# Optimization experiments

Measured on AMD Instinct MI355X. Metric: run time of the kernel, lower is better.

## Reference

```python
import jax, jax.numpy as jnp
import numpy as np

N_NODES = 50000
N_EDGES = 800000
D = 64           # node feature / hidden dim for all 5 GCN layers
NUM_GRAPHS = 512
FINAL_NEURON = 128
OUT_DIM = 1
NUM_LAYERS = 5


def setup_inputs() -> dict:
    key = jax.random.key(0)
    ks = jax.random.split(key, 20)
    inp = {}
    inp["x"] = jax.random.normal(ks[0], (N_NODES, D), dtype=jnp.float32)
    inp["edge_index"] = jax.random.randint(ks[1], (2, N_EDGES), 0, N_NODES)
    inp["batch"] = jnp.sort(jax.random.randint(ks[2], (N_NODES,), 0, NUM_GRAPHS))
    # GCNConv weights (Glorot-ish) and biases for 5 layers, all D->D
    for i in range(NUM_LAYERS):
        inp[f"W{i+1}"] = jax.random.normal(ks[3 + i], (D, D), dtype=jnp.float32) / np.sqrt(D)
        inp[f"b{i+1}"] = jnp.zeros((D,), dtype=jnp.float32)
    inp["fc1_W"] = jax.random.normal(ks[10], (D, FINAL_NEURON), dtype=jnp.float32) / np.sqrt(D)
    inp["fc1_b"] = jnp.zeros((FINAL_NEURON,), dtype=jnp.float32)
    inp["fc2_W"] = jax.random.normal(ks[11], (FINAL_NEURON, OUT_DIM), dtype=jnp.float32) / np.sqrt(FINAL_NEURON)
    inp["fc2_b"] = jnp.zeros((OUT_DIM,), dtype=jnp.float32)
    return inp


def _gcn_conv(h, src, dst, dinv, W, b):
    # PyG GCNConv: x' = D^{-1/2} (A + I) D^{-1/2} (h W) + b, deg includes self-loop
    hw = h @ W                                           # [N, D_out]
    norm_e = dinv[src] * dinv[dst]                       # [E]
    msg = hw[src] * norm_e[:, None]                      # gather + scale
    agg = jax.ops.segment_sum(msg, dst, num_segments=h.shape[0])
    agg = agg + (dinv * dinv)[:, None] * hw              # self-loop contribution
    return agg + b


def reference(x, edge_index, batch, W1, b1, W2, b2, W3, b3, W4, b4, W5, b5,
              fc1_W, fc1_b, fc2_W, fc2_b):
    src, dst = edge_index[0], edge_index[1]
    n = x.shape[0]
    # degree on A + I (in-degree at dst, plus 1 self-loop)
    deg = jax.ops.segment_sum(jnp.ones(src.shape[0], x.dtype), dst, num_segments=n) + 1.0
    dinv = jax.lax.rsqrt(deg)
    h = x
    for W, b in ((W1, b1), (W2, b2), (W3, b3), (W4, b4), (W5, b5)):
        h = jax.nn.relu(_gcn_conv(h, src, dst, dinv, W, b))
    # global_add_pool readout over graph ids
    g = jax.ops.segment_sum(h, batch, num_segments=NUM_GRAPHS)   # [G, D]
    g = jax.nn.relu(g @ fc1_W + fc1_b)
    return g @ fc2_W + fc2_b                                     # [G, 1]
```

## Files before the change

### kernel.cpp

```cpp
#include <hip/hip_runtime.h>
#include <hip/hip_fp16.h>

#define N_NODES 50000
#define N_EDGES 800000
#define D 64
#define NUM_GRAPHS 512
#define FINAL_NEURON 128
#define SCAN_NB ((N_NODES + 255) / 256)

#define BN 32
#define NB_GEMM ((N_NODES + BN - 1) / BN)
#define NB_EDGE ((N_EDGES + 255) / 256)
#define ZS 72
#define WS 72

typedef unsigned short ushort_t;
typedef _Float16 f16;
typedef __attribute__((ext_vector_type(8))) _Float16 f16x8;
typedef __attribute__((ext_vector_type(4))) float f32x4;

__device__ __forceinline__ float2 h2f(unsigned v) {
    __half2 h = *reinterpret_cast<__half2*>(&v);
    return __half22float2(h);
}

__device__ __forceinline__ void acc_add8(float4& a0, float4& a1, uint4 u) {
    float2 p;
    p = h2f(u.x); a0.x += p.x; a0.y += p.y;
    p = h2f(u.y); a0.z += p.x; a0.w += p.y;
    p = h2f(u.z); a1.x += p.x; a1.y += p.y;
    p = h2f(u.w); a1.z += p.x; a1.w += p.y;
}

__global__ void k_zero1(int* a, int n) {
    int i = blockIdx.x * blockDim.x + threadIdx.x;
    if (i < n) a[i] = 0;
}

__global__ void k_hist(const int* __restrict__ dst, int* cnt, ushort_t* __restrict__ epos) {
    int e = blockIdx.x * blockDim.x + threadIdx.x;
    if (e < N_EDGES) epos[e] = (ushort_t)atomicAdd(&cnt[dst[e]], 1);
}

__global__ void k_blocksum(const int* __restrict__ cnt, int* __restrict__ bsum,
                           float* __restrict__ dinv, float* __restrict__ g) {
    __shared__ int sdata[256];
    int t = threadIdx.x;
    int i = blockIdx.x * 256 + t;
    int v = (i < N_NODES) ? cnt[i] : 0;
    if (i < N_NODES) dinv[i] = rsqrtf((float)v + 1.0f);
    if (i < NUM_GRAPHS * D) g[i] = 0.f;
    sdata[t] = v;
    __syncthreads();
    for (int s = 128; s > 0; s >>= 1) {
        if (t < s) sdata[t] += sdata[t + s];
        __syncthreads();
    }
    if (t == 0) bsum[blockIdx.x] = sdata[0];
}

__global__ void k_scanbsum(const int* __restrict__ bsum, int* __restrict__ boff) {
    __shared__ int buf[256];
    int t = threadIdx.x;
    int v = (t < SCAN_NB) ? bsum[t] : 0;
    buf[t] = v;
    __syncthreads();
    for (int off = 1; off < 256; off <<= 1) {
        int a = (t >= off) ? buf[t - off] : 0;
        __syncthreads();
        buf[t] += a;
        __syncthreads();
    }
    if (t < SCAN_NB) boff[t] = buf[t] - v;
}

__global__ void k_localscan(const int* __restrict__ cnt, const int* __restrict__ boff,
                            int* __restrict__ row) {
    __shared__ int buf[256];
    int t = threadIdx.x;
    int i = blockIdx.x * 256 + t;
    int v = (i < N_NODES) ? cnt[i] : 0;
    buf[t] = v;
    __syncthreads();
    for (int off = 1; off < 256; off <<= 1) {
        int a = (t >= off) ? buf[t - off] : 0;
        __syncthreads();
        buf[t] += a;
        __syncthreads();
    }
    if (i < N_NODES) row[i] = boff[blockIdx.x] + buf[t] - v;
    if (i == 0) row[N_NODES] = N_EDGES;
}

__device__ __forceinline__ void stage_wT(const float* __restrict__ W,
                                         f16* WhiT, f16* WloT, int t) {
    for (int idx = t; idx < D * D; idx += 256) {
        int k = idx >> 6, j = idx & 63;
        float w = W[idx];
        f16 hi = (f16)w;
        f16 lo = (f16)(w - (float)hi);
        WhiT[j * WS + k] = hi;
        WloT[j * WS + k] = lo;
    }
}

__device__ __forceinline__ void gather_node(const int* __restrict__ row,
                                            const ushort_t* __restrict__ esrc,
                                            const uint4* __restrict__ hp,
                                            int n, int q, float4& a0, float4& a1) {
    int e = row[n], e1 = row[n + 1];
    acc_add8(a0, a1, hp[(size_t)n * 8 + q]);
    if (e + 4 <= e1) {
        int i0 = __builtin_nontemporal_load(esrc + e);
        int i1 = __builtin_nontemporal_load(esrc + e + 1);
        int i2 = __builtin_nontemporal_load(esrc + e + 2);
        int i3 = __builtin_nontemporal_load(esrc + e + 3);
        do {
            uint4 u0 = hp[(size_t)i0 * 8 + q];
            uint4 u1 = hp[(size_t)i1 * 8 + q];
            uint4 u2 = hp[(size_t)i2 * 8 + q];
            uint4 u3 = hp[(size_t)i3 * 8 + q];
            e += 4;
            i0 = __builtin_nontemporal_load(esrc + e);
            i1 = __builtin_nontemporal_load(esrc + e + 1);
            i2 = __builtin_nontemporal_load(esrc + e + 2);
            i3 = __builtin_nontemporal_load(esrc + e + 3);
            acc_add8(a0, a1, u0); acc_add8(a0, a1, u1);
            acc_add8(a0, a1, u2); acc_add8(a0, a1, u3);
        } while (e + 4 <= e1);
    }
    for (; e < e1; ++e) {
        int s = __builtin_nontemporal_load(esrc + e);
        acc_add8(a0, a1, hp[(size_t)s * 8 + q]);
    }
}

__device__ __forceinline__ void gemm_32x64(const f16* zsh, const f16* WhiT, const f16* WloT,
                                           const float* dinvsh, f16* ysh, int t) {
    int w = t >> 6, l = t & 63;
    int rt = (w >> 1) * 16;
    int cb = (w & 1) * 32;
    int lr = l & 15, lg = l >> 4;
    f32x4 acc0 = {0.f, 0.f, 0.f, 0.f}, acc1 = {0.f, 0.f, 0.f, 0.f};
#pragma unroll
    for (int ks = 0; ks < 2; ++ks) {
        f16x8 a   = *(const f16x8*)&zsh [(rt + lr)      * ZS + ks * 32 + lg * 8];
        f16x8 bh0 = *(const f16x8*)&WhiT[(cb + lr)      * WS + ks * 32 + lg * 8];
        f16x8 bl0 = *(const f16x8*)&WloT[(cb + lr)      * WS + ks * 32 + lg * 8];
        f16x8 bh1 = *(const f16x8*)&WhiT[(cb + 16 + lr) * WS + ks * 32 + lg * 8];
        f16x8 bl1 = *(const f16x8*)&WloT[(cb + 16 + lr) * WS + ks * 32 + lg * 8];
        acc0 = __builtin_amdgcn_mfma_f32_16x16x32_f16(a, bh0, acc0, 0, 0, 0);
        acc0 = __builtin_amdgcn_mfma_f32_16x16x32_f16(a, bl0, acc0, 0, 0, 0);
        acc1 = __builtin_amdgcn_mfma_f32_16x16x32_f16(a, bh1, acc1, 0, 0, 0);
        acc1 = __builtin_amdgcn_mfma_f32_16x16x32_f16(a, bl1, acc1, 0, 0, 0);
    }
#pragma unroll
    for (int r = 0; r < 4; ++r) {
        int rrow = rt + lg * 4 + r;
        float s = dinvsh[rrow];
        ysh[rrow * ZS + cb + lr]      = (f16)(acc0[r] * s);
        ysh[rrow * ZS + cb + 16 + lr] = (f16)(acc1[r] * s);
    }
}

__global__ __launch_bounds__(256, 5)
void k_transform0(const float* __restrict__ x, const float* __restrict__ dinv,
                  const float* __restrict__ W1, __half* __restrict__ hout,
                  const int* __restrict__ src, const int* __restrict__ dst,
                  const int* __restrict__ row, const ushort_t* __restrict__ epos,
                  ushort_t* __restrict__ esrc) {
    int t = threadIdx.x;
    if (blockIdx.x >= NB_GEMM) {
        int e = (blockIdx.x - NB_GEMM) * 256 + t;
        if (e < N_EDGES) esrc[row[dst[e]] + (int)epos[e]] = (ushort_t)src[e];
        return;
    }
    __shared__ __attribute__((aligned(16))) f16 WhiT[D * WS];
    __shared__ __attribute__((aligned(16))) f16 WloT[D * WS];
    __shared__ __attribute__((aligned(16))) f16 zsh[BN * ZS];
    __shared__ __attribute__((aligned(16))) f16 ysh[BN * ZS];
    __shared__ float dinvsh[BN];
    int base = blockIdx.x * BN;
    stage_wT(W1, WhiT, WloT, t);
    if (t < BN) dinvsh[t] = (base + t < N_NODES) ? dinv[base + t] : 0.f;

    int nl = t >> 3, q = t & 7;
    int n = base + nl;
    float4 xa = {0,0,0,0}, xb = {0,0,0,0};
    if (n < N_NODES) {
        xa = ((const float4*)x)[(size_t)n * 16 + q * 2];
        xb = ((const float4*)x)[(size_t)n * 16 + q * 2 + 1];
    }
    f16x8 zv;
    zv[0] = (f16)xa.x; zv[1] = (f16)xa.y; zv[2] = (f16)xa.z; zv[3] = (f16)xa.w;
    zv[4] = (f16)xb.x; zv[5] = (f16)xb.y; zv[6] = (f16)xb.z; zv[7] = (f16)xb.w;
    *(f16x8*)&zsh[nl * ZS + q * 8] = zv;
    __syncthreads();
    gemm_32x64(zsh, WhiT, WloT, dinvsh, ysh, t);
    __syncthreads();
    if (n < N_NODES) {
        uint4 o = *(const uint4*)&ysh[nl * ZS + q * 8];
        ((uint4*)hout)[(size_t)n * 8 + q] = o;
    }
}

__global__ __launch_bounds__(256, 5)
void k_layer(const int* __restrict__ row, const ushort_t* __restrict__ esrc,
             const __half* __restrict__ hin, const float* __restrict__ dinv,
             const float* __restrict__ bias, const float* __restrict__ Wn,
             __half* __restrict__ hout) {
    __shared__ __attribute__((aligned(16))) f16 WhiT[D * WS];
    __shared__ __attribute__((aligned(16))) f16 WloT[D * WS];
    __shared__ __attribute__((aligned(16))) f16 zsh[BN * ZS];
    __shared__ __attribute__((aligned(16))) f16 ysh[BN * ZS];
    __shared__ float dinvsh[BN];
    int t = threadIdx.x;
    int base = blockIdx.x * BN;
    stage_wT(Wn, WhiT, WloT, t);
    if (t < BN) dinvsh[t] = (base + t < N_NODES) ? dinv[base + t] : 0.f;

    int nl = t >> 3, q = t & 7;
    int n = base + nl;
    float4 a0 = {0,0,0,0}, a1 = {0,0,0,0};
    float s = 0.f;
    if (n < N_NODES) {
        gather_node(row, esrc, (const uint4*)hin, n, q, a0, a1);
        s = dinv[n];
    }
    float4 b0 = ((const float4*)bias)[2 * q];
    float4 b1 = ((const float4*)bias)[2 * q + 1];
    f16x8 zv;
    zv[0] = (f16)fmaxf(a0.x * s + b0.x, 0.f);
    zv[1] = (f16)fmaxf(a0.y * s + b0.y, 0.f);
    zv[2] = (f16)fmaxf(a0.z * s + b0.z, 0.f);
    zv[3] = (f16)fmaxf(a0.w * s + b0.w, 0.f);
    zv[4] = (f16)fmaxf(a1.x * s + b1.x, 0.f);
    zv[5] = (f16)fmaxf(a1.y * s + b1.y, 0.f);
    zv[6] = (f16)fmaxf(a1.z * s + b1.z, 0.f);
    zv[7] = (f16)fmaxf(a1.w * s + b1.w, 0.f);
    *(f16x8*)&zsh[nl * ZS + q * 8] = zv;
    __syncthreads();
    gemm_32x64(zsh, WhiT, WloT, dinvsh, ysh, t);
    __syncthreads();
    if (n < N_NODES) {
        uint4 o = *(const uint4*)&ysh[nl * ZS + q * 8];
        ((uint4*)hout)[(size_t)n * 8 + q] = o;
    }
}

__global__ __launch_bounds__(256, 8)
void k_layer_pool(const int* __restrict__ row, const ushort_t* __restrict__ esrc,
                  const __half* __restrict__ hin, const float* __restrict__ dinv,
                  const float* __restrict__ bias, const int* __restrict__ batch,
                  float* __restrict__ g) {
    __shared__ float zf[BN * 65];
    __shared__ int bsh[BN];
    int t = threadIdx.x;
    int base = blockIdx.x * BN;
    if (t < BN) bsh[t] = (base + t < N_NODES) ? batch[base + t] : -1;

    int nl = t >> 3, q = t & 7;
    int n = base + nl;
    float4 a0 = {0,0,0,0}, a1 = {0,0,0,0};
    float s = 0.f;
    if (n < N_NODES) {
        gather_node(row, esrc, (const uint4*)hin, n, q, a0, a1);
        s = dinv[n];
    }
    float4 b0 = ((const float4*)bias)[2 * q];
    float4 b1 = ((const float4*)bias)[2 * q + 1];
    float* zr = &zf[nl * 65 + q * 8];
    zr[0] = fmaxf(a0.x * s + b0.x, 0.f);
    zr[1] = fmaxf(a0.y * s + b0.y, 0.f);
    zr[2] = fmaxf(a0.z * s + b0.z, 0.f);
    zr[3] = fmaxf(a0.w * s + b0.w, 0.f);
    zr[4] = fmaxf(a1.x * s + b1.x, 0.f);
    zr[5] = fmaxf(a1.y * s + b1.y, 0.f);
    zr[6] = fmaxf(a1.z * s + b1.z, 0.f);
    zr[7] = fmaxf(a1.w * s + b1.w, 0.f);
    __syncthreads();
    int f = t & 63, grp = t >> 6;
    int n0 = grp * 8;
    int cur = bsh[n0];
    float acc = 0.f;
#pragma unroll
    for (int k2 = 0; k2 < 8; ++k2) {
        int bb = bsh[n0 + k2];
        if (bb < 0) break;
        if (bb != cur) { atomicAdd(&g[cur * D + f], acc); acc = 0.f; cur = bb; }
        acc += zf[(n0 + k2) * 65 + f];
    }
    if (cur >= 0) atomicAdd(&g[cur * D + f], acc);
}

__global__ void k_mlp(const float* __restrict__ g, const float* __restrict__ W1,
                      const float* __restrict__ b1, const float* __restrict__ W2,
                      const float* __restrict__ b2, float* __restrict__ out) {
    __shared__ float red[FINAL_NEURON];
    int row = blockIdx.x;
    int j = threadIdx.x;
    float acc = 0.f;
#pragma unroll
    for (int k = 0; k < D; ++k) acc += g[row * D + k] * W1[k * FINAL_NEURON + j];
    acc = fmaxf(acc + b1[j], 0.f);
    red[j] = acc * W2[j];
    __syncthreads();
    for (int s = 64; s > 0; s >>= 1) {
        if (j < s) red[j] += red[j + s];
        __syncthreads();
    }
    if (j == 0) out[row] = red[0] + b2[0];
}

extern "C" void kernel_launch(void* const* d_in, const int* in_sizes, int n_in,
                              void* d_out, int out_size, void* d_ws, size_t ws_size,
                              hipStream_t stream) {
    const float* x     = (const float*)d_in[0];
    const int*   ei    = (const int*)d_in[1];
    const int*   src   = ei;
    const int*   dst   = ei + N_EDGES;
    const int*   batch = (const int*)d_in[2];
    const float* W[5]  = {(const float*)d_in[3], (const float*)d_in[5], (const float*)d_in[7],
                          (const float*)d_in[9], (const float*)d_in[11]};
    const float* b[5]  = {(const float*)d_in[4], (const float*)d_in[6], (const float*)d_in[8],
                          (const float*)d_in[10], (const float*)d_in[12]};
    const float* fc1W  = (const float*)d_in[13];
    const float* fc1b  = (const float*)d_in[14];
    const float* fc2W  = (const float*)d_in[15];
    const float* fc2b  = (const float*)d_in[16];
    float* out = (float*)d_out;

    __half*   yA   = (__half*)d_ws;
    __half*   yB   = yA + (size_t)N_NODES * D;
    float*    g    = (float*)(yB + (size_t)N_NODES * D);
    float*    dinv = g + NUM_GRAPHS * D;
    int*      cnt  = (int*)(dinv + N_NODES);
    int*      row  = cnt + N_NODES;
    int*      bsum = row + N_NODES + 1;
    int*      boff = bsum + 256;
    ushort_t* epos = (ushort_t*)(boff + 256);
    ushort_t* esrc = epos + N_EDGES;

    k_zero1<<<(N_NODES + 255) / 256, 256, 0, stream>>>(cnt, N_NODES);
    k_hist<<<(N_EDGES + 255) / 256, 256, 0, stream>>>(dst, cnt, epos);
    k_blocksum<<<SCAN_NB, 256, 0, stream>>>(cnt, bsum, dinv, g);
    k_scanbsum<<<1, 256, 0, stream>>>(bsum, boff);
    k_localscan<<<SCAN_NB, 256, 0, stream>>>(cnt, boff, row);

    k_transform0<<<NB_GEMM + NB_EDGE, 256, 0, stream>>>(x, dinv, W[0], yA,
                                                        src, dst, row, epos, esrc);

    k_layer<<<NB_GEMM, 256, 0, stream>>>(row, esrc, yA, dinv, b[0], W[1], yB);
    k_layer<<<NB_GEMM, 256, 0, stream>>>(row, esrc, yB, dinv, b[1], W[2], yA);
    k_layer<<<NB_GEMM, 256, 0, stream>>>(row, esrc, yA, dinv, b[2], W[3], yB);
    k_layer<<<NB_GEMM, 256, 0, stream>>>(row, esrc, yB, dinv, b[3], W[4], yA);

    k_layer_pool<<<NB_GEMM, 256, 0, stream>>>(row, esrc, yA, dinv, b[4], batch, g);

    k_mlp<<<NUM_GRAPHS, FINAL_NEURON, 0, stream>>>(g, fc1W, fc1b, fc2W, fc2b, out);
}
```

Before: 272.8 us.

## Halve node tile, split gather across two lanes, pre-split weights once

The node tile per block shrinks from 32 to 16 rows. Each node's edge gather is now split across two 8-lane groups that interleave edges and combine their partial sums with a shuffle. The fp16 hi/lo transposed weight split for all five layers is computed once in a prep kernel, so each block only copies the prepared weights into LDS instead of converting fp32 weights itself. Bounds checks are dropped because 50000 divides evenly by 16. The goal is more memory-level parallelism in the gather and less per-block setup, at the cost of twice as many blocks each reloading the weight tiles.

```diff
diff --git a/kernel.cpp b/kernel.cpp
--- a/kernel.cpp
+++ b/kernel.cpp
@@ -8,16 +8,20 @@
 #define FINAL_NEURON 128
 #define SCAN_NB ((N_NODES + 255) / 256)
 
-#define BN 32
-#define NB_GEMM ((N_NODES + BN - 1) / BN)
+#define BN 16
+#define NB_GEMM (N_NODES / BN)
 #define NB_EDGE ((N_EDGES + 255) / 256)
 #define ZS 72
 #define WS 72
+#define WELEM (D * WS)
 
 typedef unsigned short ushort_t;
 typedef _Float16 f16;
+typedef __attribute__((ext_vector_type(4))) _Float16 f16x4;
 typedef __attribute__((ext_vector_type(8))) _Float16 f16x8;
 typedef __attribute__((ext_vector_type(4))) float f32x4;
+
+struct WPtrs { const float* w[5]; };
 
 __device__ __forceinline__ float2 h2f(unsigned v) {
     __half2 h = *reinterpret_cast<__half2*>(&v);
@@ -32,9 +36,24 @@
     p = h2f(u.w); a1.z += p.x; a1.w += p.y;
 }
 
-__global__ void k_zero1(int* a, int n) {
-    int i = blockIdx.x * blockDim.x + threadIdx.x;
-    if (i < n) a[i] = 0;
+__global__ void k_zero_prep(int* cnt, WPtrs wp, f16* __restrict__ whi, f16* __restrict__ wlo) {
+    int b = blockIdx.x;
+    if (b < SCAN_NB) {
+        int i = b * 256 + threadIdx.x;
+        if (i < N_NODES) cnt[i] = 0;
+        return;
+    }
+    int l = b - SCAN_NB;
+    const float* W = wp.w[l];
+    f16* hi = whi + l * WELEM;
+    f16* lo = wlo + l * WELEM;
+    for (int idx = threadIdx.x; idx < D * D; idx += 256) {
+        int k = idx >> 6, j = idx & 63;
+        float w = W[idx];
+        f16 h = (f16)w;
+        hi[j * WS + k] = h;
+        lo[j * WS + k] = (f16)(w - (float)h);
+    }
 }
 
 __global__ void k_hist(const int* __restrict__ dst, int* cnt, ushort_t* __restrict__ epos) {
@@ -92,80 +111,78 @@
     if (i == 0) row[N_NODES] = N_EDGES;
 }
 
-__device__ __forceinline__ void stage_wT(const float* __restrict__ W,
-                                         f16* WhiT, f16* WloT, int t) {
-    for (int idx = t; idx < D * D; idx += 256) {
-        int k = idx >> 6, j = idx & 63;
-        float w = W[idx];
-        f16 hi = (f16)w;
-        f16 lo = (f16)(w - (float)hi);
-        WhiT[j * WS + k] = hi;
-        WloT[j * WS + k] = lo;
-    }
-}
-
-__device__ __forceinline__ void gather_node(const int* __restrict__ row,
-                                            const ushort_t* __restrict__ esrc,
-                                            const uint4* __restrict__ hp,
-                                            int n, int q, float4& a0, float4& a1) {
-    int e = row[n], e1 = row[n + 1];
-    acc_add8(a0, a1, hp[(size_t)n * 8 + q]);
-    if (e + 4 <= e1) {
-        int i0 = __builtin_nontemporal_load(esrc + e);
-        int i1 = __builtin_nontemporal_load(esrc + e + 1);
-        int i2 = __builtin_nontemporal_load(esrc + e + 2);
-        int i3 = __builtin_nontemporal_load(esrc + e + 3);
-        do {
-            uint4 u0 = hp[(size_t)i0 * 8 + q];
-            uint4 u1 = hp[(size_t)i1 * 8 + q];
-            uint4 u2 = hp[(size_t)i2 * 8 + q];
-            uint4 u3 = hp[(size_t)i3 * 8 + q];
-            e += 4;
-            i0 = __builtin_nontemporal_load(esrc + e);
-            i1 = __builtin_nontemporal_load(esrc + e + 1);
-            i2 = __builtin_nontemporal_load(esrc + e + 2);
-            i3 = __builtin_nontemporal_load(esrc + e + 3);
-            acc_add8(a0, a1, u0); acc_add8(a0, a1, u1);
-            acc_add8(a0, a1, u2); acc_add8(a0, a1, u3);
-        } while (e + 4 <= e1);
-    }
-    for (; e < e1; ++e) {
+__device__ __forceinline__ void stage_w_lds(const f16* __restrict__ whi_g,
+                                            const f16* __restrict__ wlo_g,
+                                            f16* WhiT, f16* WloT, int t) {
+    const uint4* sh = (const uint4*)whi_g;
+    const uint4* sl = (const uint4*)wlo_g;
+    uint4* dh = (uint4*)WhiT;
+    uint4* dl = (uint4*)WloT;
+#pragma unroll 3
+    for (int i = 0; i < 3; ++i) {
+        int idx = t + i * 256;
+        if (idx < WELEM / 8) { dh[idx] = sh[idx]; dl[idx] = sl[idx]; }
+    }
+}
+
+__device__ __forceinline__ void gather_node16(const int* __restrict__ row,
+                                              const ushort_t* __restrict__ esrc,
+                                              const uint4* __restrict__ hp,
+                                              int n, int g, int q, float4& a0, float4& a1) {
+    int e = row[n] + g, e1 = row[n + 1];
+    if (g == 0) acc_add8(a0, a1, hp[(size_t)n * 8 + q]);
+    int i0 = __builtin_nontemporal_load(esrc + e);
+    int i1 = __builtin_nontemporal_load(esrc + e + 2);
+    int i2 = __builtin_nontemporal_load(esrc + e + 4);
+    int i3 = __builtin_nontemporal_load(esrc + e + 6);
+    while (e + 6 < e1) {
+        uint4 u0 = hp[(size_t)i0 * 8 + q];
+        uint4 u1 = hp[(size_t)i1 * 8 + q];
+        uint4 u2 = hp[(size_t)i2 * 8 + q];
+        uint4 u3 = hp[(size_t)i3 * 8 + q];
+        e += 8;
+        i0 = __builtin_nontemporal_load(esrc + e);
+        i1 = __builtin_nontemporal_load(esrc + e + 2);
+        i2 = __builtin_nontemporal_load(esrc + e + 4);
+        i3 = __builtin_nontemporal_load(esrc + e + 6);
+        acc_add8(a0, a1, u0); acc_add8(a0, a1, u1);
+        acc_add8(a0, a1, u2); acc_add8(a0, a1, u3);
+    }
+    for (; e < e1; e += 2) {
         int s = __builtin_nontemporal_load(esrc + e);
         acc_add8(a0, a1, hp[(size_t)s * 8 + q]);
     }
 }
 
-__device__ __forceinline__ void gemm_32x64(const f16* zsh, const f16* WhiT, const f16* WloT,
-                                           const float* dinvsh, f16* ysh, int t) {
+__device__ __forceinline__ void gemm_16x64(f16* zsh, const f16* WhiT, const f16* WloT,
+                                           const float* dinvsh, int t) {
     int w = t >> 6, l = t & 63;
-    int rt = (w >> 1) * 16;
-    int cb = (w & 1) * 32;
+    int cb = w * 16;
     int lr = l & 15, lg = l >> 4;
-    f32x4 acc0 = {0.f, 0.f, 0.f, 0.f}, acc1 = {0.f, 0.f, 0.f, 0.f};
-#pragma unroll
-    for (int ks = 0; ks < 2; ++ks) {
-        f16x8 a   = *(const f16x8*)&zsh [(rt + lr)      * ZS + ks * 32 + lg * 8];
-        f16x8 bh0 = *(const f16x8*)&WhiT[(cb + lr)      * WS + ks * 32 + lg * 8];
-        f16x8 bl0 = *(const f16x8*)&WloT[(cb + lr)      * WS + ks * 32 + lg * 8];
-        f16x8 bh1 = *(const f16x8*)&WhiT[(cb + 16 + lr) * WS + ks * 32 + lg * 8];
-        f16x8 bl1 = *(const f16x8*)&WloT[(cb + 16 + lr) * WS + ks * 32 + lg * 8];
-        acc0 = __builtin_amdgcn_mfma_f32_16x16x32_f16(a, bh0, acc0, 0, 0, 0);
-        acc0 = __builtin_amdgcn_mfma_f32_16x16x32_f16(a, bl0, acc0, 0, 0, 0);
-        acc1 = __builtin_amdgcn_mfma_f32_16x16x32_f16(a, bh1, acc1, 0, 0, 0);
-        acc1 = __builtin_amdgcn_mfma_f32_16x16x32_f16(a, bl1, acc1, 0, 0, 0);
-    }
+    f32x4 acc = {0.f, 0.f, 0.f, 0.f};
+    f16x8 a0  = *(const f16x8*)&zsh[lr * ZS + lg * 8];
+    f16x8 a1  = *(const f16x8*)&zsh[lr * ZS + 32 + lg * 8];
+    f16x8 bh0 = *(const f16x8*)&WhiT[(cb + lr) * WS + lg * 8];
+    f16x8 bl0 = *(const f16x8*)&WloT[(cb + lr) * WS + lg * 8];
+    f16x8 bh1 = *(const f16x8*)&WhiT[(cb + lr) * WS + 32 + lg * 8];
+    f16x8 bl1 = *(const f16x8*)&WloT[(cb + lr) * WS + 32 + lg * 8];
+    acc = __builtin_amdgcn_mfma_f32_16x16x32_f16(a0, bh0, acc, 0, 0, 0);
+    acc = __builtin_amdgcn_mfma_f32_16x16x32_f16(a0, bl0, acc, 0, 0, 0);
+    acc = __builtin_amdgcn_mfma_f32_16x16x32_f16(a1, bh1, acc, 0, 0, 0);
+    acc = __builtin_amdgcn_mfma_f32_16x16x32_f16(a1, bl1, acc, 0, 0, 0);
+    __syncthreads();
 #pragma unroll
     for (int r = 0; r < 4; ++r) {
-        int rrow = rt + lg * 4 + r;
+        int rrow = lg * 4 + r;
         float s = dinvsh[rrow];
-        ysh[rrow * ZS + cb + lr]      = (f16)(acc0[r] * s);
-        ysh[rrow * ZS + cb + 16 + lr] = (f16)(acc1[r] * s);
-    }
-}
-
-__global__ __launch_bounds__(256, 5)
+        zsh[rrow * ZS + cb + lr] = (f16)(acc[r] * s);
+    }
+}
+
+__global__ __launch_bounds__(256, 6)
 void k_transform0(const float* __restrict__ x, const float* __restrict__ dinv,
-                  const float* __restrict__ W1, __half* __restrict__ hout,
+                  const f16* __restrict__ whi_g, const f16* __restrict__ wlo_g,
+                  __half* __restrict__ hout,
                   const int* __restrict__ src, const int* __restrict__ dst,
                   const int* __restrict__ row, const ushort_t* __restrict__ epos,
                   ushort_t* __restrict__ esrc) {
@@ -175,122 +192,123 @@
         if (e < N_EDGES) esrc[row[dst[e]] + (int)epos[e]] = (ushort_t)src[e];
         return;
     }
-    __shared__ __attribute__((aligned(16))) f16 WhiT[D * WS];
-    __shared__ __attribute__((aligned(16))) f16 WloT[D * WS];
+    __shared__ __attribute__((aligned(16))) f16 WhiT[WELEM];
+    __shared__ __attribute__((aligned(16))) f16 WloT[WELEM];
     __shared__ __attribute__((aligned(16))) f16 zsh[BN * ZS];
-    __shared__ __attribute__((aligned(16))) f16 ysh[BN * ZS];
     __shared__ float dinvsh[BN];
     int base = blockIdx.x * BN;
-    stage_wT(W1, WhiT, WloT, t);
-    if (t < BN) dinvsh[t] = (base + t < N_NODES) ? dinv[base + t] : 0.f;
-
-    int nl = t >> 3, q = t & 7;
-    int n = base + nl;
-    float4 xa = {0,0,0,0}, xb = {0,0,0,0};
-    if (n < N_NODES) {
-        xa = ((const float4*)x)[(size_t)n * 16 + q * 2];
-        xb = ((const float4*)x)[(size_t)n * 16 + q * 2 + 1];
-    }
-    f16x8 zv;
-    zv[0] = (f16)xa.x; zv[1] = (f16)xa.y; zv[2] = (f16)xa.z; zv[3] = (f16)xa.w;
-    zv[4] = (f16)xb.x; zv[5] = (f16)xb.y; zv[6] = (f16)xb.z; zv[7] = (f16)xb.w;
-    *(f16x8*)&zsh[nl * ZS + q * 8] = zv;
-    __syncthreads();
-    gemm_32x64(zsh, WhiT, WloT, dinvsh, ysh, t);
-    __syncthreads();
-    if (n < N_NODES) {
-        uint4 o = *(const uint4*)&ysh[nl * ZS + q * 8];
-        ((uint4*)hout)[(size_t)n * 8 + q] = o;
-    }
-}
-
-__global__ __launch_bounds__(256, 5)
+    stage_w_lds(whi_g, wlo_g, WhiT, WloT, t);
+    if (t < BN) dinvsh[t] = dinv[base + t];
+
+    int nl = t >> 4, c4 = t & 15;
+    float4 xv = ((const float4*)x)[(size_t)(base + nl) * 16 + c4];
+    f16x4 zv = {(f16)xv.x, (f16)xv.y, (f16)xv.z, (f16)xv.w};
+    *(f16x4*)&zsh[nl * ZS + c4 * 4] = zv;
+    __syncthreads();
+    gemm_16x64(zsh, WhiT, WloT, dinvsh, t);
+    __syncthreads();
+    if (t < 128) {
+        int n2 = t >> 3, q = t & 7;
+        uint4 o = *(const uint4*)&zsh[n2 * ZS + q * 8];
+        ((uint4*)hout)[(size_t)(base + n2) * 8 + q] = o;
+    }
+}
+
+__global__ __launch_bounds__(256, 6)
 void k_layer(const int* __restrict__ row, const ushort_t* __restrict__ esrc,
              const __half* __restrict__ hin, const float* __restrict__ dinv,
-             const float* __restrict__ bias, const float* __restrict__ Wn,
+             const float* __restrict__ bias,
+             const f16* __restrict__ whi_g, const f16* __restrict__ wlo_g,
              __half* __restrict__ hout) {
-    __shared__ __attribute__((aligned(16))) f16 WhiT[D * WS];
-    __shared__ __attribute__((aligned(16))) f16 WloT[D * WS];
+    __shared__ __attribute__((aligned(16))) f16 WhiT[WELEM];
+    __shared__ __attribute__((aligned(16))) f16 WloT[WELEM];
     __shared__ __attribute__((aligned(16))) f16 zsh[BN * ZS];
-    __shared__ __attribute__((aligned(16))) f16 ysh[BN * ZS];
     __shared__ float dinvsh[BN];
     int t = threadIdx.x;
     int base = blockIdx.x * BN;
-    stage_wT(Wn, WhiT, WloT, t);
-    if (t < BN) dinvsh[t] = (base + t < N_NODES) ? dinv[base + t] : 0.f;
-
-    int nl = t >> 3, q = t & 7;
+    stage_w_lds(whi_g, wlo_g, WhiT, WloT, t);
+    if (t < BN) dinvsh[t] = dinv[base + t];
+
+    int nl = t >> 4, m = t & 15, g = m >> 3, q = m & 7;
     int n = base + nl;
     float4 a0 = {0,0,0,0}, a1 = {0,0,0,0};
-    float s = 0.f;
-    if (n < N_NODES) {
-        gather_node(row, esrc, (const uint4*)hin, n, q, a0, a1);
-        s = dinv[n];
-    }
+    gather_node16(row, esrc, (const uint4*)hin, n, g, q, a0, a1);
+    a0.x += __shfl_xor(a0.x, 8); a0.y += __shfl_xor(a0.y, 8);
+    a0.z += __shfl_xor(a0.z, 8); a0.w += __shfl_xor(a0.w, 8);
+    a1.x += __shfl_xor(a1.x, 8); a1.y += __shfl_xor(a1.y, 8);
+    a1.z += __shfl_xor(a1.z, 8); a1.w += __shfl_xor(a1.w, 8);
+    float s = dinv[n];
     float4 b0 = ((const float4*)bias)[2 * q];
     float4 b1 = ((const float4*)bias)[2 * q + 1];
-    f16x8 zv;
-    zv[0] = (f16)fmaxf(a0.x * s + b0.x, 0.f);
-    zv[1] = (f16)fmaxf(a0.y * s + b0.y, 0.f);
-    zv[2] = (f16)fmaxf(a0.z * s + b0.z, 0.f);
-    zv[3] = (f16)fmaxf(a0.w * s + b0.w, 0.f);
-    zv[4] = (f16)fmaxf(a1.x * s + b1.x, 0.f);
-    zv[5] = (f16)fmaxf(a1.y * s + b1.y, 0.f);
-    zv[6] = (f16)fmaxf(a1.z * s + b1.z, 0.f);
-    zv[7] = (f16)fmaxf(a1.w * s + b1.w, 0.f);
-    *(f16x8*)&zsh[nl * ZS + q * 8] = zv;
-    __syncthreads();
-    gemm_32x64(zsh, WhiT, WloT, dinvsh, ysh, t);
-    __syncthreads();
-    if (n < N_NODES) {
-        uint4 o = *(const uint4*)&ysh[nl * ZS + q * 8];
-        ((uint4*)hout)[(size_t)n * 8 + q] = o;
-    }
-}
-
-__global__ __launch_bounds__(256, 8)
+    if (g == 0) {
+        f16x8 zv;
+        zv[0] = (f16)fmaxf(a0.x * s + b0.x, 0.f);
+        zv[1] = (f16)fmaxf(a0.y * s + b0.y, 0.f);
+        zv[2] = (f16)fmaxf(a0.z * s + b0.z, 0.f);
+        zv[3] = (f16)fmaxf(a0.w * s + b0.w, 0.f);
+        zv[4] = (f16)fmaxf(a1.x * s + b1.x, 0.f);
+        zv[5] = (f16)fmaxf(a1.y * s + b1.y, 0.f);
+        zv[6] = (f16)fmaxf(a1.z * s + b1.z, 0.f);
+        zv[7] = (f16)fmaxf(a1.w * s + b1.w, 0.f);
+        *(f16x8*)&zsh[nl * ZS + q * 8] = zv;
+    }
+    __syncthreads();
+    gemm_16x64(zsh, WhiT, WloT, dinvsh, t);
+    __syncthreads();
+    if (t < 128) {
+        int n2 = t >> 3, q2 = t & 7;
+        uint4 o = *(const uint4*)&zsh[n2 * ZS + q2 * 8];
+        ((uint4*)hout)[(size_t)(base + n2) * 8 + q2] = o;
+    }
+}
+
+__global__ __launch_bounds__(256, 6)
 void k_layer_pool(const int* __restrict__ row, const ushort_t* __restrict__ esrc,
                   const __half* __restrict__ hin, const float* __restrict__ dinv,
                   const float* __restrict__ bias, const int* __restrict__ batch,
                   float* __restrict__ g) {
-    __shared__ float zf[BN * 65];
+    __shared__ float zf[BN * 68];
     __shared__ int bsh[BN];
     int t = threadIdx.x;
     int base = blockIdx.x * BN;
-    if (t < BN) bsh[t] = (base + t < N_NODES) ? batch[base + t] : -1;
-
-    int nl = t >> 3, q = t & 7;
+    if (t < BN) bsh[t] = batch[base + t];
+
+    int nl = t >> 4, m = t & 15, g2 = m >> 3, q = m & 7;
     int n = base + nl;
     float4 a0 = {0,0,0,0}, a1 = {0,0,0,0};
-    float s = 0.f;
-    if (n < N_NODES) {
-        gather_node(row, esrc, (const uint4*)hin, n, q, a0, a1);
-        s = dinv[n];
-    }
+    gather_node16(row, esrc, (const uint4*)hin, n, g2, q, a0, a1);
+    a0.x += __shfl_xor(a0.x, 8); a0.y += __shfl_xor(a0.y, 8);
+    a0.z += __shfl_xor(a0.z, 8); a0.w += __shfl_xor(a0.w, 8);
+    a1.x += __shfl_xor(a1.x, 8); a1.y += __shfl_xor(a1.y, 8);
+    a1.z += __shfl_xor(a1.z, 8); a1.w += __shfl_xor(a1.w, 8);
+    float s = dinv[n];
     float4 b0 = ((const float4*)bias)[2 * q];
     float4 b1 = ((const float4*)bias)[2 * q + 1];
-    float* zr = &zf[nl * 65 + q * 8];
-    zr[0] = fmaxf(a0.x * s + b0.x, 0.f);
-    zr[1] = fmaxf(a0.y * s + b0.y, 0.f);
-    zr[2] = fmaxf(a0.z * s + b0.z, 0.f);
-    zr[3] = fmaxf(a0.w * s + b0.w, 0.f);
-    zr[4] = fmaxf(a1.x * s + b1.x, 0.f);
-    zr[5] = fmaxf(a1.y * s + b1.y, 0.f);
-    zr[6] = fmaxf(a1.z * s + b1.z, 0.f);
-    zr[7] = fmaxf(a1.w * s + b1.w, 0.f);
+    if (g2 == 0) {
+        float4 r0, r1;
+        r0.x = fmaxf(a0.x * s + b0.x, 0.f);
+        r0.y = fmaxf(a0.y * s + b0.y, 0.f);
+        r0.z = fmaxf(a0.z * s + b0.z, 0.f);
+        r0.w = fmaxf(a0.w * s + b0.w, 0.f);
+        r1.x = fmaxf(a1.x * s + b1.x, 0.f);
+        r1.y = fmaxf(a1.y * s + b1.y, 0.f);
+        r1.z = fmaxf(a1.z * s + b1.z, 0.f);
+        r1.w = fmaxf(a1.w * s + b1.w, 0.f);
+        *(float4*)&zf[nl * 68 + q * 8]     = r0;
+        *(float4*)&zf[nl * 68 + q * 8 + 4] = r1;
+    }
     __syncthreads();
     int f = t & 63, grp = t >> 6;
-    int n0 = grp * 8;
+    int n0 = grp * 4;
     int cur = bsh[n0];
     float acc = 0.f;
 #pragma unroll
-    for (int k2 = 0; k2 < 8; ++k2) {
+    for (int k2 = 0; k2 < 4; ++k2) {
         int bb = bsh[n0 + k2];
-        if (bb < 0) break;
         if (bb != cur) { atomicAdd(&g[cur * D + f], acc); acc = 0.f; cur = bb; }
-        acc += zf[(n0 + k2) * 65 + f];
-    }
-    if (cur >= 0) atomicAdd(&g[cur * D + f], acc);
+        acc += zf[(n0 + k2) * 68 + f];
+    }
+    atomicAdd(&g[cur * D + f], acc);
 }
 
 __global__ void k_mlp(const float* __restrict__ g, const float* __restrict__ W1,
@@ -320,8 +338,10 @@
     const int*   src   = ei;
     const int*   dst   = ei + N_EDGES;
     const int*   batch = (const int*)d_in[2];
-    const float* W[5]  = {(const float*)d_in[3], (const float*)d_in[5], (const float*)d_in[7],
-                          (const float*)d_in[9], (const float*)d_in[11]};
+    WPtrs wp;
+    wp.w[0] = (const float*)d_in[3];  wp.w[1] = (const float*)d_in[5];
+    wp.w[2] = (const float*)d_in[7];  wp.w[3] = (const float*)d_in[9];
+    wp.w[4] = (const float*)d_in[11];
     const float* b[5]  = {(const float*)d_in[4], (const float*)d_in[6], (const float*)d_in[8],
                           (const float*)d_in[10], (const float*)d_in[12]};
     const float* fc1W  = (const float*)d_in[13];
@@ -332,7 +352,9 @@
 
     __half*   yA   = (__half*)d_ws;
     __half*   yB   = yA + (size_t)N_NODES * D;
-    float*    g    = (float*)(yB + (size_t)N_NODES * D);
+    f16*      whiG = (f16*)(yB + (size_t)N_NODES * D);
+    f16*      wloG = whiG + 5 * WELEM;
+    float*    g    = (float*)(wloG + 5 * WELEM);
     float*    dinv = g + NUM_GRAPHS * D;
     int*      cnt  = (int*)(dinv + N_NODES);
     int*      row  = cnt + N_NODES;
@@ -341,19 +363,23 @@
     ushort_t* epos = (ushort_t*)(boff + 256);
     ushort_t* esrc = epos + N_EDGES;
 
-    k_zero1<<<(N_NODES + 255) / 256, 256, 0, stream>>>(cnt, N_NODES);
+    k_zero_prep<<<SCAN_NB + 5, 256, 0, stream>>>(cnt, wp, whiG, wloG);
     k_hist<<<(N_EDGES + 255) / 256, 256, 0, stream>>>(dst, cnt, epos);
     k_blocksum<<<SCAN_NB, 256, 0, stream>>>(cnt, bsum, dinv, g);
     k_scanbsum<<<1, 256, 0, stream>>>(bsum, boff);
     k_localscan<<<SCAN_NB, 256, 0, stream>>>(cnt, boff, row);
 
-    k_transform0<<<NB_GEMM + NB_EDGE, 256, 0, stream>>>(x, dinv, W[0], yA,
+    k_transform0<<<NB_GEMM + NB_EDGE, 256, 0, stream>>>(x, dinv, whiG, wloG, yA,
                                                         src, dst, row, epos, esrc);
 
-    k_layer<<<NB_GEMM, 256, 0, stream>>>(row, esrc, yA, dinv, b[0], W[1], yB);
-    k_layer<<<NB_GEMM, 256, 0, stream>>>(row, esrc, yB, dinv, b[1], W[2], yA);
-    k_layer<<<NB_GEMM, 256, 0, stream>>>(row, esrc, yA, dinv, b[2], W[3], yB);
-    k_layer<<<NB_GEMM, 256, 0, stream>>>(row, esrc, yB, dinv, b[3], W[4], yA);
+    k_layer<<<NB_GEMM, 256, 0, stream>>>(row, esrc, yA, dinv, b[0],
+                                         whiG + 1 * WELEM, wloG + 1 * WELEM, yB);
+    k_layer<<<NB_GEMM, 256, 0, stream>>>(row, esrc, yB, dinv, b[1],
+                                         whiG + 2 * WELEM, wloG + 2 * WELEM, yA);
+    k_layer<<<NB_GEMM, 256, 0, stream>>>(row, esrc, yA, dinv, b[2],
+                                         whiG + 3 * WELEM, wloG + 3 * WELEM, yB);
+    k_layer<<<NB_GEMM, 256, 0, stream>>>(row, esrc, yB, dinv, b[3],
+                                         whiG + 4 * WELEM, wloG + 4 * WELEM, yA);
 
     k_layer_pool<<<NB_GEMM, 256, 0, stream>>>(row, esrc, yA, dinv, b[4], batch, g);
 
```

Result: faster. 262.8 us (-3.7%).
